# Kernel tuning notes

Measured on AMD Instinct MI355X. Metric: run time of the kernel, lower is better.

## Reference

```python
import jax, jax.numpy as jnp
import numpy as np

K = 3          # conv kernel size
STRIDE = 1     # conv stride (SAME padding)
ITERS = 3      # DR routing iterations
EPS = 1e-9     # squash epsilon


def squash(s, axis):
    # v = ||s||^2 / (1 + ||s||^2) * s / ||s||   (DR squash)
    sq = jnp.sum(s * s, axis=axis, keepdims=True)
    return (sq / (1.0 + sq)) * s * jax.lax.rsqrt(sq + EPS)


def setup_inputs() -> dict:
    key = jax.random.key(0)
    k1, k2, k3 = jax.random.split(key, 3)
    b, h, w, iCaps, iPose = 8, 12, 12, 32, 16
    oCaps, oPose = 32, 16
    x = jax.random.normal(k1, (b, h, w, iCaps, iPose), dtype=jnp.float32)
    # Wa: [kk*iCaps, oCaps, iPose, oPose] (leading 1 of the TF weight is dropped)
    fan = K * K * iCaps * iPose
    W = jax.random.normal(k2, (K * K * iCaps, oCaps, iPose, oPose), dtype=jnp.float32) * np.float32(np.sqrt(2.0 / fan))
    # biases: [oCaps, oPose] (TF shape [1,1,oCaps,oPose,1], broadcastable)
    biases = jax.random.normal(k3, (oCaps, oPose), dtype=jnp.float32) * 0.05
    return {"x": x, "W": W, "biases": biases}


def _kernel_tile(x2d):
    # im2col for SAME padding, stride 1.  x2d: (b, h, w, C) -> (b, h, w, k*k, C)
    b, h, w, C = x2d.shape
    pad = K // 2
    xp = jnp.pad(x2d, ((0, 0), (pad, pad), (pad, pad), (0, 0)))
    patches = jnp.stack(
        [xp[:, i:i + h, j:j + w, :] for i in range(K) for j in range(K)], axis=3
    )
    return patches  # (b, h, w, k*k, C)


def reference(x, W, biases):
    b, h, w, iCaps, iPose = x.shape
    iC = K * K * iCaps
    oC, oP = biases.shape

    # 1. kernel_tile: gather k*k neighborhoods
    patches = _kernel_tile(x.reshape(b, h, w, iCaps * iPose))      # (b,h,w,kk,iCaps*iPose)
    u = patches.reshape(b * h * w, iC, iPose)                       # (bx, iC, iPose)

    # 2. transform_view (vector capsules): votes[n,i,c,:] = u[n,i,:] @ W[i,c,:,:]
    votes = jnp.einsum('nip,icpq->nicq', u, W)                      # (bx, iC, oC, oP)

    # 3. DR routing
    bx = votes.shape[0]
    logits = jnp.zeros((bx, iC, oC), dtype=votes.dtype)
    v = None
    for ii in range(ITERS):
        c = jax.nn.softmax(logits, axis=2)                          # coupling coeffs over oCaps
        s = jnp.einsum('nic,nicq->ncq', c, votes) + biases          # (bx, oC, oP)
        v = squash(s, axis=2)
        if ii < ITERS - 1:
            logits = logits + jnp.einsum('nicq,ncq->nic', votes, v)  # agreement

    return v.reshape(b, h, w, oC, oP)
```

## Files before the change

kernel.cpp:

```cpp
#include <hip/hip_runtime.h>
#include <stdint.h>

typedef unsigned short ushort_t;

#define KK3 3
#define IC 32
#define IP 16
#define OC 32
#define OP 16
#define NI 288
#define HH 12
#define WWW 12
#define NTOT 1152
#define CQ 512
#define EPSQ 1e-9f
#define RWAVES 4
#define RSTEPS 36
#define NIP 144
#define NIG 18
#define IPG 8

typedef __attribute__((ext_vector_type(8))) short bf16x8;
typedef __attribute__((ext_vector_type(4))) float f32x4;

__device__ __forceinline__ float bf_lo(unsigned u) { return __uint_as_float(u << 16); }
__device__ __forceinline__ float bf_hi(unsigned u) { return __uint_as_float(u & 0xffff0000u); }
__device__ __forceinline__ ushort_t f2bf(float f) {
    unsigned u = __float_as_uint(f);
    return (ushort_t)((u + 0x7fffu + ((u >> 16) & 1u)) >> 16);
}

__global__ __launch_bounds__(64) void pack_kernel(
    const float* __restrict__ W, ushort_t* __restrict__ Wp)
{
    const int blk = blockIdx.x;
    const int ip = blk >> 5;
    const int c = blk & 31;
    const int l = threadIdx.x;
    const int i = ip * 2 + ((l >> 5) & 1);
    const int p0 = ((l >> 4) & 1) * 8;
    const int q = l & 15;
    const float* src = W + (((size_t)(i * 32 + c) * 16 + p0) * 16 + q);
    union { ushort_t s[8]; uint4 u4; } o;
#pragma unroll
    for (int j = 0; j < 8; ++j) o.s[j] = f2bf(src[(size_t)j * 16]);
    *(uint4*)(Wp + ((size_t)blk * 64 + l) * 8) = o.u4;
}

__global__ __launch_bounds__(256) void votes_s0_kernel(
    const float* __restrict__ x, const ushort_t* __restrict__ Wp,
    ushort_t* __restrict__ votes, float* __restrict__ s0_part,
    int nStart, int nCount)
{
    const int t = threadIdx.x;
    const int w = t >> 6;
    const int l = t & 63;
    const int pxt = blockIdx.x;
    const int ig = blockIdx.y;

    const int pxa = pxt * 16 + (l & 15);
    const int n = nStart + ((pxa < nCount) ? pxa : 0);
    const int b = n / (HH * WWW);
    const int rem = n % (HH * WWW);
    const int y = rem / WWW;
    const int xx = rem % WWW;
    const int ioff = (l >> 5) & 1;
    const int p0 = ((l >> 4) & 1) * 8;

    const int q = l & 15;
    const int r0 = (l >> 4) * 4;

    const bf16x8 z8 = {0, 0, 0, 0, 0, 0, 0, 0};
    const f32x4 z4 = {0.f, 0.f, 0.f, 0.f};

    f32x4 accs0[8];
#pragma unroll
    for (int ctl = 0; ctl < 8; ++ctl) accs0[ctl] = z4;

    for (int m = 0; m < IPG; ++m) {
        const int ip = ig * IPG + m;
        union { ushort_t s[8]; bf16x8 v; } ua;
        {
            const int i = ip * 2 + ioff;
            const int ky = i / (KK3 * IC);
            const int kx = (i / IC) % KK3;
            const int ic = i & (IC - 1);
            const int sy = y + ky - 1;
            const int sx = xx + kx - 1;
            if (sy >= 0 && sy < HH && sx >= 0 && sx < WWW) {
                const float* s = x + ((((size_t)b * HH + sy) * WWW + sx) * IC + ic) * IP + p0;
                const float4 v0 = *(const float4*)s;
                const float4 v1 = *(const float4*)(s + 4);
                ua.s[0] = f2bf(v0.x); ua.s[1] = f2bf(v0.y); ua.s[2] = f2bf(v0.z); ua.s[3] = f2bf(v0.w);
                ua.s[4] = f2bf(v1.x); ua.s[5] = f2bf(v1.y); ua.s[6] = f2bf(v1.z); ua.s[7] = f2bf(v1.w);
            } else {
#pragma unroll
                for (int j = 0; j < 8; ++j) ua.s[j] = 0;
            }
        }
        ushort_t* be_ptr[4];
        ushort_t* bo_ptr[4];
#pragma unroll
        for (int r = 0; r < 4; ++r) {
            const size_t nl = (size_t)(pxt * 16 + r0 + r);
            be_ptr[r] = votes + (nl * NI + 2 * ip) * CQ + w * 128 + q;
            bo_ptr[r] = be_ptr[r] + CQ;
        }
        const bool rowOK = (pxt * 16 + r0 + 3 < nCount) | (nCount % 16 == 0);

#pragma unroll
        for (int ctl = 0; ctl < 8; ++ctl) {
            const int ct = w * 8 + ctl;
            const bf16x8 frag = *(const bf16x8*)(Wp + (((size_t)ip * 32 + ct) * 64 + l) * 8);
            const bf16x8 be = (l < 32) ? frag : z8;
            const bf16x8 bo = (l < 32) ? z8 : frag;
            const f32x4 ve = __builtin_amdgcn_mfma_f32_16x16x32_bf16(ua.v, be, z4, 0, 0, 0);
            const f32x4 vo = __builtin_amdgcn_mfma_f32_16x16x32_bf16(ua.v, bo, z4, 0, 0, 0);
            accs0[ctl] = __builtin_amdgcn_mfma_f32_16x16x32_bf16(ua.v, frag, accs0[ctl], 0, 0, 0);
            if (rowOK) {
#pragma unroll
                for (int r = 0; r < 4; ++r) {
                    be_ptr[r][ctl * 16] = f2bf(ve[r]);
                    bo_ptr[r][ctl * 16] = f2bf(vo[r]);
                }
            }
        }
    }

    {
#pragma unroll
        for (int ctl = 0; ctl < 8; ++ctl) {
            const int cq = (w * 8 + ctl) * 16 + q;
#pragma unroll
            for (int r = 0; r < 4; ++r) {
                const int px = pxt * 16 + r0 + r;
                if (px < nCount)
                    s0_part[((size_t)ig * nCount + px) * CQ + cq] = accs0[ctl][r];
            }
        }
    }
}

__global__ __launch_bounds__(256) void s0_fin_kernel(
    const float* __restrict__ s0_part, float* __restrict__ s0_pre,
    int nStart, int nCount)
{
    const int bn = blockIdx.x;
    const int t = threadIdx.x;
#pragma unroll
    for (int rep = 0; rep < 2; ++rep) {
        const int k = t + rep * 256;
        float s = 0.f;
#pragma unroll
        for (int g = 0; g < NIG; ++g)
            s += s0_part[((size_t)g * nCount + bn) * CQ + k];
        s0_pre[(size_t)(nStart + bn) * CQ + k] = s;
    }
}

#define UNPACK16(A, B)                                                     \
    const float f0 = bf_lo(A.x), f1 = bf_hi(A.x), f2 = bf_lo(A.y),         \
                f3 = bf_hi(A.y), f4 = bf_lo(A.z), f5 = bf_hi(A.z),         \
                f6 = bf_lo(A.w), f7 = bf_hi(A.w), f8 = bf_lo(B.x),         \
                f9 = bf_hi(B.x), f10 = bf_lo(B.y), f11 = bf_hi(B.y),       \
                f12 = bf_lo(B.z), f13 = bf_hi(B.z), f14 = bf_lo(B.w),      \
                f15 = bf_hi(B.w);

__global__ __launch_bounds__(256) void route_kernel(
    const ushort_t* __restrict__ votes, const float* __restrict__ s0_pre,
    const float* __restrict__ bias, float* __restrict__ out, int nStart)
{
    __shared__ float lg_lds[NI * OC];
    __shared__ float sPart[RWAVES][CQ];
    __shared__ float s_sh[CQ];
    __shared__ float v_sh[CQ];
    __shared__ float fac_sh[OC];

    const int bn = blockIdx.x;
    const int t = threadIdx.x;
    const int wv = t >> 6;
    const int l = t & 63;
    const int isub = l >> 5;
    const int c = l & 31;
    const int iBase = 2 * wv + isub;

    const ushort_t* pbase = votes + (size_t)bn * NI * CQ + (size_t)iBase * CQ + c * OP;
    const size_t stepB = (size_t)8 * CQ;

#pragma unroll
    for (int rep = 0; rep < 2; ++rep) {
        const int k = t + rep * 256;
        s_sh[k] = fmaf(s0_pre[(size_t)(nStart + bn) * CQ + k], 1.0f / OC, bias[k]);
    }
    __syncthreads();
    if (t < OC) {
        float sq = 0.f;
#pragma unroll
        for (int q = 0; q < OP; ++q) { const float s = s_sh[t * OP + q]; sq = fmaf(s, s, sq); }
        fac_sh[t] = (sq / (1.0f + sq)) * rsqrtf(sq + EPSQ);
    }
    __syncthreads();
#pragma unroll
    for (int rep = 0; rep < 2; ++rep) {
        const int k = t + rep * 256;
        v_sh[k] = s_sh[k] * fac_sh[k >> 4];
    }
    __syncthreads();

    float sa[16];
    float vr[16];

#define RBODY(AA, BB, rr)                                                   \
        {                                                                   \
            UNPACK16(AA, BB)                                                \
            float a = f0 * vr[0];                                           \
            a = fmaf(f1, vr[1], a);   a = fmaf(f2, vr[2], a);               \
            a = fmaf(f3, vr[3], a);   a = fmaf(f4, vr[4], a);               \
            a = fmaf(f5, vr[5], a);   a = fmaf(f6, vr[6], a);               \
            a = fmaf(f7, vr[7], a);   a = fmaf(f8, vr[8], a);               \
            a = fmaf(f9, vr[9], a);   a = fmaf(f10, vr[10], a);             \
            a = fmaf(f11, vr[11], a); a = fmaf(f12, vr[12], a);             \
            a = fmaf(f13, vr[13], a); a = fmaf(f14, vr[14], a);             \
            a = fmaf(f15, vr[15], a);                                       \
            const int li = (iBase + 8 * (rr)) * OC + c;                     \
            if (it == 0) lg_lds[li] = a;                                    \
            else          a += lg_lds[li];                                  \
            const float e = __expf(a);                                      \
            float es = e;                                                   \
            es += __shfl_xor(es, 1);                                        \
            es += __shfl_xor(es, 2);                                        \
            es += __shfl_xor(es, 4);                                        \
            es += __shfl_xor(es, 8);                                        \
            es += __shfl_xor(es, 16);                                       \
            const float coup = __fdividef(e, es);                           \
            sa[0] = fmaf(coup, f0, sa[0]);   sa[1] = fmaf(coup, f1, sa[1]); \
            sa[2] = fmaf(coup, f2, sa[2]);   sa[3] = fmaf(coup, f3, sa[3]); \
            sa[4] = fmaf(coup, f4, sa[4]);   sa[5] = fmaf(coup, f5, sa[5]); \
            sa[6] = fmaf(coup, f6, sa[6]);   sa[7] = fmaf(coup, f7, sa[7]); \
            sa[8] = fmaf(coup, f8, sa[8]);   sa[9] = fmaf(coup, f9, sa[9]); \
            sa[10] = fmaf(coup, f10, sa[10]); sa[11] = fmaf(coup, f11, sa[11]); \
            sa[12] = fmaf(coup, f12, sa[12]); sa[13] = fmaf(coup, f13, sa[13]); \
            sa[14] = fmaf(coup, f14, sa[14]); sa[15] = fmaf(coup, f15, sa[15]); \
        }
#define RPREF(AA, BB, rn)                                                   \
        if ((rn) < RSTEPS) {                                                \
            const uint4* pn = (const uint4*)(pbase + (size_t)(rn) * stepB); \
            AA = pn[0]; BB = pn[1];                                         \
        }

#pragma unroll
    for (int it = 0; it < 2; ++it) {
#pragma unroll
        for (int k = 0; k < 4; ++k) {
            const float4 v4 = *(const float4*)&v_sh[c * 16 + 4 * k];
            vr[4*k] = v4.x; vr[4*k+1] = v4.y; vr[4*k+2] = v4.z; vr[4*k+3] = v4.w;
        }
#pragma unroll
        for (int q = 0; q < 16; ++q) sa[q] = 0.f;

        uint4 A0, B0, A1, B1, A2, B2, A3, B3, A4, B4, A5, B5;
        RPREF(A0, B0, 0)
        RPREF(A1, B1, 1)
        RPREF(A2, B2, 2)
        RPREF(A3, B3, 3)
        RPREF(A4, B4, 4)
        RPREF(A5, B5, 5)
        for (int r = 0; r < RSTEPS; r += 6) {
            RBODY(A0, B0, r)     RPREF(A0, B0, r + 6)
            RBODY(A1, B1, r + 1) RPREF(A1, B1, r + 7)
            RBODY(A2, B2, r + 2) RPREF(A2, B2, r + 8)
            RBODY(A3, B3, r + 3) RPREF(A3, B3, r + 9)
            RBODY(A4, B4, r + 4) RPREF(A4, B4, r + 10)
            RBODY(A5, B5, r + 5) RPREF(A5, B5, r + 11)
        }

#pragma unroll
        for (int q = 0; q < 16; ++q) sa[q] += __shfl_xor(sa[q], 32);
        if (isub == 0) {
#pragma unroll
            for (int k = 0; k < 4; ++k)
                *(float4*)&sPart[wv][c * 16 + 4 * k] = make_float4(sa[4*k], sa[4*k+1], sa[4*k+2], sa[4*k+3]);
        }
        __syncthreads();
#pragma unroll
        for (int rep = 0; rep < 2; ++rep) {
            const int k = t + rep * 256;
            float s = (sPart[0][k] + sPart[1][k]) + (sPart[2][k] + sPart[3][k]);
            s_sh[k] = s + bias[k];
        }
        __syncthreads();
        if (t < OC) {
            float sq = 0.f;
#pragma unroll
            for (int q = 0; q < OP; ++q) { const float s = s_sh[t * OP + q]; sq = fmaf(s, s, sq); }
            fac_sh[t] = (sq / (1.0f + sq)) * rsqrtf(sq + EPSQ);
        }
        __syncthreads();
#pragma unroll
        for (int rep = 0; rep < 2; ++rep) {
            const int k = t + rep * 256;
            v_sh[k] = s_sh[k] * fac_sh[k >> 4];
        }
        __syncthreads();
    }

#pragma unroll
    for (int rep = 0; rep < 2; ++rep) {
        const int k = t + rep * 256;
        out[(size_t)(nStart + bn) * CQ + k] = v_sh[k];
    }
}

extern "C" void kernel_launch(void* const* d_in, const int* in_sizes, int n_in,
                              void* d_out, int out_size, void* d_ws, size_t ws_size,
                              hipStream_t stream)
{
    const float* x = (const float*)d_in[0];
    const float* Wg = (const float*)d_in[1];
    const float* bias = (const float*)d_in[2];
    float* out = (float*)d_out;

    const size_t perN = (size_t)NI * CQ * sizeof(ushort_t);
    const size_t packBytes = (size_t)NIP * 32 * 64 * 8 * 2;
    const size_t s0Bytes = (size_t)NTOT * CQ * sizeof(float);
    const size_t perNpart = (size_t)NIG * CQ * sizeof(float);

    int chunk = 768;
    if (ws_size < (size_t)chunk * (perN + perNpart) + packBytes + s0Bytes) {
        size_t avail = (ws_size > packBytes + s0Bytes) ? ws_size - packBytes - s0Bytes : 0;
        chunk = (int)(avail / (perN + perNpart));
        chunk &= ~15;
        if (chunk < 16) chunk = 16;
    }
    const size_t packOff = (size_t)chunk * perN;
    const size_t s0Off = packOff + packBytes;
    const size_t partOff = s0Off + s0Bytes;

    ushort_t* votes = (ushort_t*)d_ws;
    ushort_t* Wp = (ushort_t*)((char*)d_ws + packOff);
    float* s0_pre = (float*)((char*)d_ws + s0Off);
    float* s0_part = (float*)((char*)d_ws + partOff);

    hipLaunchKernelGGL(pack_kernel, dim3(NIP * 32), dim3(64), 0, stream, Wg, Wp);

    for (int start = 0; start < NTOT; start += chunk) {
        const int cnt = (NTOT - start < chunk) ? (NTOT - start) : chunk;
        hipLaunchKernelGGL(votes_s0_kernel, dim3((cnt + 15) / 16, NIG), dim3(256), 0, stream,
                           x, Wp, votes, s0_part, start, cnt);
        hipLaunchKernelGGL(s0_fin_kernel, dim3(cnt), dim3(256), 0, stream,
                           s0_part, s0_pre, start, cnt);
        hipLaunchKernelGGL(route_kernel, dim3(cnt), dim3(256), 0, stream,
                           votes, s0_pre, bias, out, start);
    }
}
```

Measured before the change: 250.0 us.

## Stage vote stores through LDS for coalesced writes and fuse s0 reduction into routing

Vote tiles from the MFMA outputs are first written to a per-wave shared-memory slab and then stored to global memory as 16-byte vectors, replacing scattered 2-byte stores. The separate s0_fin kernel is removed and its partial-sum reduction moves into the start of route_kernel, which drops one launch and the s0_pre buffer. Tail handling for chunk sizes that are not multiples of 16 is also removed. Chunks that are not 16-aligned would now be handled incorrectly, and the extra LDS use may lower occupancy.

```diff
diff --git a/kernel.cpp b/kernel.cpp
--- a/kernel.cpp
+++ b/kernel.cpp
@@ -19,6 +19,9 @@
 #define NIP 144
 #define NIG 18
 #define IPG 8
+#define SROW 132
+#define SPAR (16 * SROW)
+#define SWAVE (2 * SPAR)
 
 typedef __attribute__((ext_vector_type(8))) short bf16x8;
 typedef __attribute__((ext_vector_type(4))) float f32x4;
@@ -52,14 +55,15 @@
     ushort_t* __restrict__ votes, float* __restrict__ s0_part,
     int nStart, int nCount)
 {
+    __shared__ ushort_t slab[4 * SWAVE];
+
     const int t = threadIdx.x;
     const int w = t >> 6;
     const int l = t & 63;
     const int pxt = blockIdx.x;
     const int ig = blockIdx.y;
 
-    const int pxa = pxt * 16 + (l & 15);
-    const int n = nStart + ((pxa < nCount) ? pxa : 0);
+    const int n = nStart + pxt * 16 + (l & 15);
     const int b = n / (HH * WWW);
     const int rem = n % (HH * WWW);
     const int y = rem / WWW;
@@ -69,6 +73,10 @@
 
     const int q = l & 15;
     const int r0 = (l >> 4) * 4;
+    const int j16 = l & 15;
+    const int g4 = l >> 4;
+
+    ushort_t* const myslab = slab + w * SWAVE;
 
     const bf16x8 z8 = {0, 0, 0, 0, 0, 0, 0, 0};
     const f32x4 z4 = {0.f, 0.f, 0.f, 0.f};
@@ -98,15 +106,6 @@
                 for (int j = 0; j < 8; ++j) ua.s[j] = 0;
             }
         }
-        ushort_t* be_ptr[4];
-        ushort_t* bo_ptr[4];
-#pragma unroll
-        for (int r = 0; r < 4; ++r) {
-            const size_t nl = (size_t)(pxt * 16 + r0 + r);
-            be_ptr[r] = votes + (nl * NI + 2 * ip) * CQ + w * 128 + q;
-            bo_ptr[r] = be_ptr[r] + CQ;
-        }
-        const bool rowOK = (pxt * 16 + r0 + 3 < nCount) | (nCount % 16 == 0);
 
 #pragma unroll
         for (int ctl = 0; ctl < 8; ++ctl) {
@@ -117,12 +116,25 @@
             const f32x4 ve = __builtin_amdgcn_mfma_f32_16x16x32_bf16(ua.v, be, z4, 0, 0, 0);
             const f32x4 vo = __builtin_amdgcn_mfma_f32_16x16x32_bf16(ua.v, bo, z4, 0, 0, 0);
             accs0[ctl] = __builtin_amdgcn_mfma_f32_16x16x32_bf16(ua.v, frag, accs0[ctl], 0, 0, 0);
-            if (rowOK) {
-#pragma unroll
-                for (int r = 0; r < 4; ++r) {
-                    be_ptr[r][ctl * 16] = f2bf(ve[r]);
-                    bo_ptr[r][ctl * 16] = f2bf(vo[r]);
-                }
+#pragma unroll
+            for (int r = 0; r < 4; ++r) {
+                myslab[(r0 + r) * SROW + ctl * 16 + q] = f2bf(ve[r]);
+                myslab[SPAR + (r0 + r) * SROW + ctl * 16 + q] = f2bf(vo[r]);
+            }
+        }
+
+#pragma unroll
+        for (int s = 0; s < 2; ++s) {
+#pragma unroll
+            for (int h = 0; h < 4; ++h) {
+                const int row = h * 4 + g4;
+                const ushort_t* sp = myslab + s * SPAR + row * SROW + j16 * 8;
+                const uint2 lo = *(const uint2*)sp;
+                const uint2 hi = *(const uint2*)(sp + 4);
+                ushort_t* dst = votes + ((size_t)(pxt * 16 + row) * NI + (2 * ip + s)) * CQ
+                                + w * 128 + j16 * 8;
+                uint4 o; o.x = lo.x; o.y = lo.y; o.z = hi.x; o.w = hi.y;
+                *(uint4*)dst = o;
             }
         }
     }
@@ -132,29 +144,9 @@
         for (int ctl = 0; ctl < 8; ++ctl) {
             const int cq = (w * 8 + ctl) * 16 + q;
 #pragma unroll
-            for (int r = 0; r < 4; ++r) {
-                const int px = pxt * 16 + r0 + r;
-                if (px < nCount)
-                    s0_part[((size_t)ig * nCount + px) * CQ + cq] = accs0[ctl][r];
-            }
-        }
-    }
-}
-
-__global__ __launch_bounds__(256) void s0_fin_kernel(
-    const float* __restrict__ s0_part, float* __restrict__ s0_pre,
-    int nStart, int nCount)
-{
-    const int bn = blockIdx.x;
-    const int t = threadIdx.x;
-#pragma unroll
-    for (int rep = 0; rep < 2; ++rep) {
-        const int k = t + rep * 256;
-        float s = 0.f;
-#pragma unroll
-        for (int g = 0; g < NIG; ++g)
-            s += s0_part[((size_t)g * nCount + bn) * CQ + k];
-        s0_pre[(size_t)(nStart + bn) * CQ + k] = s;
+            for (int r = 0; r < 4; ++r)
+                s0_part[((size_t)ig * nCount + pxt * 16 + r0 + r) * CQ + cq] = accs0[ctl][r];
+        }
     }
 }
 
@@ -167,8 +159,9 @@
                 f15 = bf_hi(B.w);
 
 __global__ __launch_bounds__(256) void route_kernel(
-    const ushort_t* __restrict__ votes, const float* __restrict__ s0_pre,
-    const float* __restrict__ bias, float* __restrict__ out, int nStart)
+    const ushort_t* __restrict__ votes, const float* __restrict__ s0_part,
+    const float* __restrict__ bias, float* __restrict__ out,
+    int nStart, int nCount)
 {
     __shared__ float lg_lds[NI * OC];
     __shared__ float sPart[RWAVES][CQ];
@@ -190,7 +183,11 @@
 #pragma unroll
     for (int rep = 0; rep < 2; ++rep) {
         const int k = t + rep * 256;
-        s_sh[k] = fmaf(s0_pre[(size_t)(nStart + bn) * CQ + k], 1.0f / OC, bias[k]);
+        float s = 0.f;
+#pragma unroll
+        for (int g = 0; g < NIG; ++g)
+            s += s0_part[((size_t)g * nCount + bn) * CQ + k];
+        s_sh[k] = fmaf(s, 1.0f / OC, bias[k]);
     }
     __syncthreads();
     if (t < OC) {
@@ -322,34 +319,29 @@
 
     const size_t perN = (size_t)NI * CQ * sizeof(ushort_t);
     const size_t packBytes = (size_t)NIP * 32 * 64 * 8 * 2;
-    const size_t s0Bytes = (size_t)NTOT * CQ * sizeof(float);
     const size_t perNpart = (size_t)NIG * CQ * sizeof(float);
 
     int chunk = 768;
-    if (ws_size < (size_t)chunk * (perN + perNpart) + packBytes + s0Bytes) {
-        size_t avail = (ws_size > packBytes + s0Bytes) ? ws_size - packBytes - s0Bytes : 0;
+    if (ws_size < (size_t)chunk * (perN + perNpart) + packBytes) {
+        size_t avail = (ws_size > packBytes) ? ws_size - packBytes : 0;
         chunk = (int)(avail / (perN + perNpart));
         chunk &= ~15;
         if (chunk < 16) chunk = 16;
     }
     const size_t packOff = (size_t)chunk * perN;
-    const size_t s0Off = packOff + packBytes;
-    const size_t partOff = s0Off + s0Bytes;
+    const size_t partOff = packOff + packBytes;
 
     ushort_t* votes = (ushort_t*)d_ws;
     ushort_t* Wp = (ushort_t*)((char*)d_ws + packOff);
-    float* s0_pre = (float*)((char*)d_ws + s0Off);
     float* s0_part = (float*)((char*)d_ws + partOff);
 
     hipLaunchKernelGGL(pack_kernel, dim3(NIP * 32), dim3(64), 0, stream, Wg, Wp);
 
     for (int start = 0; start < NTOT; start += chunk) {
         const int cnt = (NTOT - start < chunk) ? (NTOT - start) : chunk;
-        hipLaunchKernelGGL(votes_s0_kernel, dim3((cnt + 15) / 16, NIG), dim3(256), 0, stream,
+        hipLaunchKernelGGL(votes_s0_kernel, dim3(cnt / 16, NIG), dim3(256), 0, stream,
                            x, Wp, votes, s0_part, start, cnt);
-        hipLaunchKernelGGL(s0_fin_kernel, dim3(cnt), dim3(256), 0, stream,
-                           s0_part, s0_pre, start, cnt);
         hipLaunchKernelGGL(route_kernel, dim3(cnt), dim3(256), 0, stream,
-                           votes, s0_pre, bias, out, start);
-    }
-}
+                           votes, s0_part, bias, out, start, cnt);
+    }
+}
```

New measurement: 249.3 us. Within noise of the previous version (-0.3%).
